# Performance work log

Measured on AMD Instinct MI355X. Metric: run time of the kernel, lower is better.

The kernel has to match this reference:

```python
import jax, jax.numpy as jnp
import numpy as np

INPUT_DIM, LATENT_DIM, HIDDEN_DIM, BATCH = 1024, 128, 1024, 32768


def setup_inputs() -> dict:
    key = jax.random.key(0)
    ks = jax.random.split(key, 12)
    s = 0.02
    x = (jax.random.uniform(ks[0], (BATCH, INPUT_DIM)) < 0.5).astype(jnp.float32)  # binary data
    eps = jax.random.normal(ks[1], (BATCH, LATENT_DIM), dtype=jnp.float32)
    return {
        "x": x,
        "eps": eps,
        "We1": jax.random.normal(ks[2], (INPUT_DIM, HIDDEN_DIM)) * s,
        "be1": jnp.zeros((HIDDEN_DIM,), jnp.float32),
        "Wmu": jax.random.normal(ks[3], (HIDDEN_DIM, LATENT_DIM)) * s,
        "bmu": jnp.zeros((LATENT_DIM,), jnp.float32),
        "Wls": jax.random.normal(ks[4], (HIDDEN_DIM, LATENT_DIM)) * s,
        "bls": jnp.zeros((LATENT_DIM,), jnp.float32),
        "Wd1": jax.random.normal(ks[5], (LATENT_DIM, HIDDEN_DIM)) * s,
        "bd1": jnp.zeros((HIDDEN_DIM,), jnp.float32),
        "Wd2": jax.random.normal(ks[6], (HIDDEN_DIM, INPUT_DIM)) * s,
        "bd2": jnp.zeros((INPUT_DIM,), jnp.float32),
    }


def reference(x, eps, We1, be1, Wmu, bmu, Wls, bls, Wd1, bd1, Wd2, bd2):
    # Encoder: one hidden ReLU layer, mu / logsigma heads
    h = jax.nn.relu(x @ We1 + be1)                      # [B, H]
    mu = h @ Wmu + bmu                                  # [B, L]
    logsigma = h @ Wls + bls                            # [B, L]
    # Reparameterization: z = sigma * eps + mu (vectorized diag(exp(logsigma)) @ eps)
    z = mu + jnp.exp(logsigma) * eps                    # [B, L]
    # Decoder: one hidden ReLU layer, sigmoid Bernoulli params
    hd = jax.nn.relu(z @ Wd1 + bd1)                     # [B, H]
    theta = jax.nn.sigmoid(hd @ Wd2 + bd2)              # [B, D]
    # Bernoulli log-likelihood: sum_j log(theta^x * (1-theta)^(1-x))
    log_px = jnp.sum(x * jnp.log(theta) + (1.0 - x) * jnp.log1p(-theta), axis=-1)  # [B]
    # KL(q||N(0,I)) = 0.5 * sum(sigma^2 + mu^2 - log(sigma^2) - 1)
    kl = 0.5 * jnp.sum(jnp.exp(2.0 * logsigma) + mu * mu - 2.0 * logsigma - 1.0, axis=-1)  # [B]
    return log_px - kl                                  # elbo_mc [B]
```

## Files before the change

### kernel.cpp

```cpp
#include <hip/hip_runtime.h>
#include <cstdint>
#include <cstddef>


typedef __bf16 bf16x8 __attribute__((ext_vector_type(8)));
typedef float f32x4 __attribute__((ext_vector_type(4)));

__device__ __forceinline__ unsigned short f32_to_bf16(float f) {
  unsigned int u = __float_as_uint(f);
  u += 0x7fffu + ((u >> 16) & 1u);
  return (unsigned short)(u >> 16);
}

struct TransJob { const float* in; unsigned short* out; int K, N, blkEnd; };

__global__ void prep_k(TransJob j0, TransJob j1, TransJob j2,
                       TransJob j3, TransJob j4,
                       const float* __restrict__ x,
                       unsigned short* __restrict__ xbf,
                       unsigned short* __restrict__ xbit,
                       int n4, int castBlocks) {
  __shared__ float tile[32][33];
  int bid = blockIdx.x;
  int tx = threadIdx.x, ty = threadIdx.y;
  if (bid >= j4.blkEnd) {
    int tid = ty * 32 + tx;
    int stride = castBlocks * 256;
    for (int i = (bid - j4.blkEnd) * 256 + tid; i < n4; i += stride) {
      float4 v = reinterpret_cast<const float4*>(x)[i];
      ushort4 o = make_ushort4(f32_to_bf16(v.x), f32_to_bf16(v.y),
                               f32_to_bf16(v.z), f32_to_bf16(v.w));
      reinterpret_cast<ushort4*>(xbf)[i] = o;
      unsigned int nib = (v.x != 0.f ? 1u : 0u) | (v.y != 0.f ? 2u : 0u) |
                         (v.z != 0.f ? 4u : 0u) | (v.w != 0.f ? 8u : 0u);
      unsigned int n1 = __shfl_down(nib, 1, 64);
      unsigned int n2 = __shfl_down(nib, 2, 64);
      unsigned int n3 = __shfl_down(nib, 3, 64);
      if ((tid & 3) == 0)
        xbit[i >> 2] = (unsigned short)(nib | (n1 << 4) | (n2 << 8) | (n3 << 12));
    }
    return;
  }
  TransJob j; int base;
  if (bid < j0.blkEnd)      { j = j0; base = 0; }
  else if (bid < j1.blkEnd) { j = j1; base = j0.blkEnd; }
  else if (bid < j2.blkEnd) { j = j2; base = j1.blkEnd; }
  else if (bid < j3.blkEnd) { j = j3; base = j2.blkEnd; }
  else                      { j = j4; base = j3.blkEnd; }
  int local = bid - base;
  int gxN = j.N >> 5;
  int n0 = (local % gxN) * 32, k0 = (local / gxN) * 32;
#pragma unroll
  for (int r = 0; r < 32; r += 8)
    tile[ty + r][tx] = j.in[(size_t)(k0 + ty + r) * j.N + n0 + tx];
  __syncthreads();
#pragma unroll
  for (int r = 0; r < 32; r += 8)
    j.out[(size_t)(n0 + ty + r) * j.K + k0 + tx] = f32_to_bf16(tile[tx][ty + r]);
}

__device__ __forceinline__ void gl_lds16(const unsigned short* g, unsigned short* l) {
  __builtin_amdgcn_global_load_lds(
      (__attribute__((address_space(1))) void*)g,
      (__attribute__((address_space(3))) void*)l, 16, 0, 0);
}

template <int EPI, int TAG>
__global__ __launch_bounds__(512, 2) void gemm256(
    const unsigned short* __restrict__ A, const unsigned short* __restrict__ BT,
    int gx, int N, int K,
    const float* __restrict__ bias0,
    unsigned short* __restrict__ outb, float* __restrict__ outf,
    const unsigned short* __restrict__ xbit) {
  __shared__ __align__(16) unsigned short lds[2][2][256 * 64];

  const int tid = threadIdx.x;
  const int lane = tid & 63;
  const int wave = tid >> 6;
  const int wr = wave >> 2;
  const int wc = wave & 3;
  const int lm = lane & 15, lq = lane >> 4;
  const int sw = lm & 7;

  const int bid = blockIdx.x;
  const int xcd = bid & 7;
  const int t8 = bid >> 3;
  const int m0 = (xcd + 8 * (t8 / gx)) * 256;
  const int n0 = (t8 % gx) * 256;
  const int NT = K >> 6;

  const unsigned short* gpA[2];
  const unsigned short* gpB[2];
  int loA[2], loB[2];
#pragma unroll
  for (int r = 0; r < 2; ++r) {
    int c = tid + 512 * r, rl = c >> 3, q8 = c & 7;
    int rowA = (rl & 63) + ((rl >> 6) << 7);
    int rowB = (rl & 31) + ((rl >> 5) << 6);
    gpA[r] = A + (size_t)(m0 + rowA) * K + (q8 ^ (rowA & 7)) * 8;
    gpB[r] = BT + (size_t)(n0 + rowB) * K + (q8 ^ (rowB & 7)) * 8;
    loA[r] = rowA * 64 + q8 * 8;
    loB[r] = rowB * 64 + q8 * 8;
  }

  auto stage = [&](int kind, int buf, int kt) {
#pragma unroll
    for (int r = 0; r < 2; ++r) {
      if (kind == 0)      gl_lds16(gpA[r] + kt * 64,          &lds[buf][0][loA[r]]);
      else if (kind == 3) gl_lds16(gpA[r] + 64 * K + kt * 64, &lds[buf][0][loA[r] + 64 * 64]);
      else if (kind == 1) gl_lds16(gpB[r] + kt * 64,          &lds[buf][1][loB[r]]);
      else                gl_lds16(gpB[r] + 32 * K + kt * 64, &lds[buf][1][loB[r] + 32 * 64]);
    }
  };

  stage(0, 0, 0); stage(1, 0, 0); stage(2, 0, 0); stage(3, 0, 0);
  stage(0, 1, 1); stage(1, 1, 1); stage(2, 1, 1);
  asm volatile("s_waitcnt vmcnt(6)" ::: "memory");
  __builtin_amdgcn_s_barrier();

  f32x4 acc[8][4] = {};

  const int aRow = (wr * 128 + lm) * 64;
  const int bRow = (wc * 64 + lm) * 64;
  const int c0 = ((0 | lq) ^ sw) * 8;
  const int c1 = ((4 | lq) ^ sw) * 8;

  for (int t = 0; t < NT; ++t) {
    const int b = t & 1;
    const unsigned short* Ab = &lds[b][0][0];
    const unsigned short* Bb = &lds[b][1][0];
    bf16x8 af[4][2], bf1[2][2], bf2[2][2];

#pragma unroll
    for (int i = 0; i < 4; ++i) {
      af[i][0] = *reinterpret_cast<const bf16x8*>(Ab + aRow + i * 1024 + c0);
      af[i][1] = *reinterpret_cast<const bf16x8*>(Ab + aRow + i * 1024 + c1);
    }
#pragma unroll
    for (int j = 0; j < 2; ++j) {
      bf1[j][0] = *reinterpret_cast<const bf16x8*>(Bb + bRow + j * 1024 + c0);
      bf1[j][1] = *reinterpret_cast<const bf16x8*>(Bb + bRow + j * 1024 + c1);
    }
    if (t + 1 < NT) stage(3, (t + 1) & 1, t + 1);
    __builtin_amdgcn_s_barrier();
    asm volatile("s_waitcnt lgkmcnt(0)" ::: "memory");
    __builtin_amdgcn_sched_barrier(0);
    __builtin_amdgcn_s_setprio(1);
#pragma unroll
    for (int s = 0; s < 2; ++s)
#pragma unroll
      for (int i = 0; i < 4; ++i)
#pragma unroll
        for (int j = 0; j < 2; ++j)
          acc[i][j] = __builtin_amdgcn_mfma_f32_16x16x32_bf16(af[i][s], bf1[j][s], acc[i][j], 0, 0, 0);
    __builtin_amdgcn_s_setprio(0);
    __builtin_amdgcn_s_barrier();

#pragma unroll
    for (int j = 0; j < 2; ++j) {
      bf2[j][0] = *reinterpret_cast<const bf16x8*>(Bb + bRow + (j + 2) * 1024 + c0);
      bf2[j][1] = *reinterpret_cast<const bf16x8*>(Bb + bRow + (j + 2) * 1024 + c1);
    }
    if (t + 2 < NT) stage(0, b, t + 2);
    __builtin_amdgcn_s_barrier();
    asm volatile("s_waitcnt lgkmcnt(0)" ::: "memory");
    __builtin_amdgcn_sched_barrier(0);
    __builtin_amdgcn_s_setprio(1);
#pragma unroll
    for (int s = 0; s < 2; ++s)
#pragma unroll
      for (int i = 0; i < 4; ++i)
#pragma unroll
        for (int j = 0; j < 2; ++j)
          acc[i][j + 2] = __builtin_amdgcn_mfma_f32_16x16x32_bf16(af[i][s], bf2[j][s], acc[i][j + 2], 0, 0, 0);
    __builtin_amdgcn_s_setprio(0);
    __builtin_amdgcn_s_barrier();

#pragma unroll
    for (int i = 0; i < 4; ++i) {
      af[i][0] = *reinterpret_cast<const bf16x8*>(Ab + aRow + (64 + i * 16) * 64 + c0);
      af[i][1] = *reinterpret_cast<const bf16x8*>(Ab + aRow + (64 + i * 16) * 64 + c1);
    }
    if (t + 2 < NT) stage(1, b, t + 2);
    __builtin_amdgcn_s_barrier();
    asm volatile("s_waitcnt lgkmcnt(0)" ::: "memory");
    __builtin_amdgcn_sched_barrier(0);
    __builtin_amdgcn_s_setprio(1);
#pragma unroll
    for (int s = 0; s < 2; ++s)
#pragma unroll
      for (int i = 0; i < 4; ++i)
#pragma unroll
        for (int j = 0; j < 2; ++j)
          acc[i + 4][j] = __builtin_amdgcn_mfma_f32_16x16x32_bf16(af[i][s], bf1[j][s], acc[i + 4][j], 0, 0, 0);
    __builtin_amdgcn_s_setprio(0);
    __builtin_amdgcn_s_barrier();

    if (t + 2 < NT) stage(2, b, t + 2);
    __builtin_amdgcn_s_barrier();
    __builtin_amdgcn_s_setprio(1);
#pragma unroll
    for (int s = 0; s < 2; ++s)
#pragma unroll
      for (int i = 0; i < 4; ++i)
#pragma unroll
        for (int j = 0; j < 2; ++j)
          acc[i + 4][j + 2] = __builtin_amdgcn_mfma_f32_16x16x32_bf16(af[i][s], bf2[j][s], acc[i + 4][j + 2], 0, 0, 0);
    __builtin_amdgcn_s_setprio(0);
    if (t + 2 < NT)      { asm volatile("s_waitcnt vmcnt(6)" ::: "memory"); }
    else if (t + 1 < NT) { asm volatile("s_waitcnt vmcnt(0)" ::: "memory"); }
    __builtin_amdgcn_s_barrier();
  }

  if (EPI == 0) {
#pragma unroll
    for (int i = 0; i < 8; ++i)
#pragma unroll
      for (int j = 0; j < 4; ++j) {
        int col = n0 + wc * 64 + j * 16 + lm;
        float bias = bias0[col];
#pragma unroll
        for (int r = 0; r < 4; ++r) {
          int row = m0 + wr * 128 + i * 16 + lq * 4 + r;
          float v = acc[i][j][r] + bias;
          outb[(size_t)row * N + col] = f32_to_bf16(fmaxf(v, 0.f));
        }
      }
  } else {
    const int wpr = N >> 4;
#pragma unroll
    for (int i = 0; i < 8; ++i) {
      float rs[4] = {0.f, 0.f, 0.f, 0.f};
#pragma unroll
      for (int j = 0; j < 4; ++j) {
        int col = n0 + wc * 64 + j * 16 + lm;
        float bias = bias0[col];
        int w16 = (col >> 4);
#pragma unroll
        for (int r = 0; r < 4; ++r) {
          int row = m0 + wr * 128 + i * 16 + lq * 4 + r;
          float l = acc[i][j][r] + bias;
          unsigned short mask = xbit[(size_t)row * wpr + w16];
          float tt = ((mask >> lm) & 1) ? -l : l;
          float sp = fmaxf(tt, 0.f) + __logf(1.f + __expf(-fabsf(tt)));
          rs[r] -= sp;
        }
      }
#pragma unroll
      for (int off = 1; off < 16; off <<= 1)
#pragma unroll
        for (int r = 0; r < 4; ++r) rs[r] += __shfl_xor(rs[r], off, 64);
      if (lm == 0) {
#pragma unroll
        for (int r = 0; r < 4; ++r)
          atomicAdd(&outf[m0 + wr * 128 + i * 16 + lq * 4 + r], rs[r]);
      }
    }
  }
}

__global__ __launch_bounds__(256, 1) void latent_fused(
    const unsigned short* A,
    const unsigned short* __restrict__ BT,
    const unsigned short* __restrict__ WD1,
    const float* __restrict__ bmu, const float* __restrict__ bls,
    const float* __restrict__ bd1,
    const float* __restrict__ eps,
    unsigned short* hd,
    float* __restrict__ out) {
  __shared__ __align__(16) unsigned short smem[65536];
  unsigned short* As0 = smem;
  unsigned short* As1 = smem + 8192;
  unsigned short* Bs0 = smem + 16384;
  unsigned short* Bs1 = smem + 32768;
  unsigned short* zs  = smem + 49152;
  unsigned short* Bs2 = smem;

  const int K = 1024;
  const int tid = threadIdx.x;
  const int lane = tid & 63;
  const int wave = tid >> 6;
  const int m0 = blockIdx.x * 128;
  const int lm = lane & 15, lq = lane >> 4;
  const int sw = lm & 7;

  const unsigned short* agp[4];
  const unsigned short* bgp[8];
#pragma unroll
  for (int r = 0; r < 4; ++r) {
    int c = tid + 256 * r;
    int row = c >> 3, q = (c & 7) ^ (row & 7);
    agp[r] = A + (size_t)(m0 + row) * K + q * 8;
  }
#pragma unroll
  for (int r = 0; r < 8; ++r) {
    int c = tid + 256 * r;
    int row = c >> 3, q = (c & 7) ^ (row & 7);
    bgp[r] = BT + (size_t)row * K + q * 8;
  }

  auto stage1 = [&](int buf, int kt) {
    unsigned short* Ad = buf ? As1 : As0;
    unsigned short* Bd = buf ? Bs1 : Bs0;
#pragma unroll
    for (int r = 0; r < 4; ++r) gl_lds16(agp[r] + kt, Ad + (tid + 256 * r) * 8);
#pragma unroll
    for (int r = 0; r < 8; ++r) gl_lds16(bgp[r] + kt, Bd + (tid + 256 * r) * 8);
  };

  f32x4 acc[2][16] = {};

  stage1(0, 0);
  __syncthreads();

  for (int t = 0; t < 16; ++t) {
    const int cur = t & 1;
    if (t + 1 < 16) stage1(cur ^ 1, (t + 1) * 64);
    const unsigned short* Ab = cur ? As1 : As0;
    const unsigned short* Bb = cur ? Bs1 : Bs0;
#pragma unroll
    for (int s = 0; s < 2; ++s) {
      const int so = ((s << 2) | lq) ^ sw;
      bf16x8 af[2];
#pragma unroll
      for (int i = 0; i < 2; ++i)
        af[i] = *reinterpret_cast<const bf16x8*>(Ab + (wave * 32 + i * 16 + lm) * 64 + so * 8);
#pragma unroll
      for (int j = 0; j < 16; ++j) {
        bf16x8 b = *reinterpret_cast<const bf16x8*>(Bb + (j * 16 + lm) * 64 + so * 8);
        acc[0][j] = __builtin_amdgcn_mfma_f32_16x16x32_bf16(af[0], b, acc[0][j], 0, 0, 0);
        acc[1][j] = __builtin_amdgcn_mfma_f32_16x16x32_bf16(af[1], b, acc[1][j], 0, 0, 0);
      }
    }
    __syncthreads();
  }

  auto stage2 = [&](int nt) {
#pragma unroll
    for (int ri = 0; ri < 16; ++ri) {
      int c = tid + 256 * ri;
      int row = c >> 4, slot = c & 15;
      int gc = slot ^ (row & 7);
      gl_lds16(WD1 + (size_t)(nt * 256 + row) * 128 + gc * 8, Bs2 + c * 8);
    }
  };
  stage2(0);

#pragma unroll
  for (int i = 0; i < 2; ++i) {
    float kl[4] = {0.f, 0.f, 0.f, 0.f};
#pragma unroll
    for (int j = 0; j < 8; ++j) {
      int dim = j * 16 + lm;
      float bm = bmu[dim], bl = bls[dim];
#pragma unroll
      for (int r = 0; r < 4; ++r) {
        int rowl = wave * 32 + i * 16 + lq * 4 + r;
        float mu = acc[i][j][r] + bm;
        float ls = acc[i][j + 8][r] + bl;
        float e = eps[(size_t)(m0 + rowl) * 128 + dim];
        float zv = fmaf(__expf(ls), e, mu);
        int chunk = (dim >> 3);
        int slot = chunk ^ (rowl & 7);
        zs[rowl * 128 + slot * 8 + (lm & 7)] = f32_to_bf16(zv);
        kl[r] += 0.5f * (__expf(2.f * ls) + mu * mu - 2.f * ls - 1.f);
      }
    }
#pragma unroll
    for (int off = 1; off < 16; off <<= 1)
#pragma unroll
      for (int r = 0; r < 4; ++r) kl[r] += __shfl_xor(kl[r], off, 64);
    if (lm == 0) {
#pragma unroll
      for (int r = 0; r < 4; ++r)
        out[m0 + wave * 32 + i * 16 + lq * 4 + r] = -kl[r];
    }
  }

  for (int nt = 0; nt < 4; ++nt) {
    asm volatile("s_waitcnt vmcnt(0)" ::: "memory");
    __syncthreads();
    f32x4 acc2[2][16] = {};
#pragma unroll
    for (int ks = 0; ks < 4; ++ks) {
      const int cks = (ks * 4 + lq) ^ (lm & 7);
      bf16x8 a0 = *reinterpret_cast<const bf16x8*>(zs + (wave * 32 + lm) * 128 + cks * 8);
      bf16x8 a1 = *reinterpret_cast<const bf16x8*>(zs + (wave * 32 + 16 + lm) * 128 + cks * 8);
#pragma unroll
      for (int j = 0; j < 16; ++j) {
        bf16x8 b = *reinterpret_cast<const bf16x8*>(Bs2 + (j * 16 + lm) * 128 + cks * 8);
        acc2[0][j] = __builtin_amdgcn_mfma_f32_16x16x32_bf16(a0, b, acc2[0][j], 0, 0, 0);
        acc2[1][j] = __builtin_amdgcn_mfma_f32_16x16x32_bf16(a1, b, acc2[1][j], 0, 0, 0);
      }
    }
    __syncthreads();
    if (nt + 1 < 4) stage2(nt + 1);
#pragma unroll
    for (int i = 0; i < 2; ++i)
#pragma unroll
      for (int j = 0; j < 16; ++j) {
        int col = nt * 256 + j * 16 + lm;
        float bias = bd1[col];
#pragma unroll
        for (int r = 0; r < 4; ++r) {
          int row = m0 + wave * 32 + i * 16 + lq * 4 + r;
          float v = acc2[i][j][r] + bias;
          hd[(size_t)row * 1024 + col] = f32_to_bf16(fmaxf(v, 0.f));
        }
      }
  }
}

extern "C" void kernel_launch(void* const* d_in, const int* in_sizes, int n_in,
                              void* d_out, int out_size, void* d_ws, size_t ws_size,
                              hipStream_t stream) {
  const float* x   = (const float*)d_in[0];
  const float* eps = (const float*)d_in[1];
  const float* We1 = (const float*)d_in[2];
  const float* be1 = (const float*)d_in[3];
  const float* Wmu = (const float*)d_in[4];
  const float* bmu = (const float*)d_in[5];
  const float* Wls = (const float*)d_in[6];
  const float* bls = (const float*)d_in[7];
  const float* Wd1 = (const float*)d_in[8];
  const float* bd1 = (const float*)d_in[9];
  const float* Wd2 = (const float*)d_in[10];
  const float* bd2 = (const float*)d_in[11];
  float* out = (float*)d_out;

  const int B = 32768, D = 1024, H = 1024, L = 128;

  char* ws = (char*)d_ws;
  size_t off = 0;
  auto alloc = [&](size_t bytes) {
    void* p = ws + off;
    off += (bytes + 255) & ~(size_t)255;
    return p;
  };
  unsigned short* xbf  = (unsigned short*)alloc((size_t)B * D * 2);
  unsigned short* xbit = (unsigned short*)alloc((size_t)B * D / 8);
  unsigned short* w1t  = (unsigned short*)alloc((size_t)H * D * 2);
  unsigned short* w2t  = (unsigned short*)alloc((size_t)256 * H * 2);
  unsigned short* wd1t = (unsigned short*)alloc((size_t)H * L * 2);
  unsigned short* wd2t = (unsigned short*)alloc((size_t)D * H * 2);
  unsigned short* h    = (unsigned short*)alloc((size_t)B * H * 2);
  unsigned short* hd   = h;

  TransJob j0{We1, w1t, D, H, 1024};
  TransJob j1{Wmu, w2t, H, L, 1152};
  TransJob j2{Wls, w2t + 128 * H, H, L, 1280};
  TransJob j3{Wd1, wd1t, L, H, 1408};
  TransJob j4{Wd2, wd2t, H, D, 2432};
  prep_k<<<2432 + 2048, dim3(32, 8), 0, stream>>>(
      j0, j1, j2, j3, j4, x, xbf, xbit, B * D / 4, 2048);

  gemm256<0, 1><<<512, 512, 0, stream>>>(
      xbf, w1t, 4, H, D, be1, h, nullptr, nullptr);
  latent_fused<<<B / 128, 256, 0, stream>>>(
      h, w2t, wd1t, bmu, bls, bd1, eps, hd, out);
  gemm256<2, 4><<<512, 512, 0, stream>>>(
      hd, wd2t, 4, D, H, bd2, nullptr, out, xbit);

  (void)in_sizes; (void)n_in; (void)out_size; (void)ws_size;
}
```

Before: 440.8 us.

## Expand bit-packed input in LDS for first GEMM instead of bf16 copy

The prep kernel no longer writes a bf16 copy of x. The first encoder GEMM instead loads the bit-packed x tile (one bit per element) into LDS once per block and expands it to bf16 0/1 values in shared memory each k-step. This removes a 64MB bf16 write plus its re-read, leaving only the compact bitmask traffic. The cost is ALU and LDS-store work for expansion inside the main loop, a single A buffer with changed wait counts, and an encoding that is only exact because x is binary.

```diff
diff --git a/kernel.cpp b/kernel.cpp
--- a/kernel.cpp
+++ b/kernel.cpp
@@ -17,7 +17,6 @@
 __global__ void prep_k(TransJob j0, TransJob j1, TransJob j2,
                        TransJob j3, TransJob j4,
                        const float* __restrict__ x,
-                       unsigned short* __restrict__ xbf,
                        unsigned short* __restrict__ xbit,
                        int n4, int castBlocks) {
   __shared__ float tile[32][33];
@@ -28,9 +27,6 @@
     int stride = castBlocks * 256;
     for (int i = (bid - j4.blkEnd) * 256 + tid; i < n4; i += stride) {
       float4 v = reinterpret_cast<const float4*>(x)[i];
-      ushort4 o = make_ushort4(f32_to_bf16(v.x), f32_to_bf16(v.y),
-                               f32_to_bf16(v.z), f32_to_bf16(v.w));
-      reinterpret_cast<ushort4*>(xbf)[i] = o;
       unsigned int nib = (v.x != 0.f ? 1u : 0u) | (v.y != 0.f ? 2u : 0u) |
                          (v.z != 0.f ? 4u : 0u) | (v.w != 0.f ? 8u : 0u);
       unsigned int n1 = __shfl_down(nib, 1, 64);
@@ -65,14 +61,14 @@
       (__attribute__((address_space(3))) void*)l, 16, 0, 0);
 }
 
-template <int EPI, int TAG>
+template <int EPI, int TAG, int ABIT>
 __global__ __launch_bounds__(512, 2) void gemm256(
     const unsigned short* __restrict__ A, const unsigned short* __restrict__ BT,
     int gx, int N, int K,
     const float* __restrict__ bias0,
     unsigned short* __restrict__ outb, float* __restrict__ outf,
     const unsigned short* __restrict__ xbit) {
-  __shared__ __align__(16) unsigned short lds[2][2][256 * 64];
+  __shared__ __align__(16) unsigned short smem[65536];
 
   const int tid = threadIdx.x;
   const int lane = tid & 63;
@@ -89,34 +85,75 @@
   const int n0 = (t8 % gx) * 256;
   const int NT = K >> 6;
 
+  unsigned short* const smemp = smem;
+  auto Abuf = [&](int b) -> unsigned short* {
+    return ABIT ? smemp : smemp + b * 32768;
+  };
+  auto Bbuf = [&](int b) -> unsigned short* {
+    return ABIT ? smemp + 16384 + b * 16384 : smemp + b * 32768 + 16384;
+  };
+
   const unsigned short* gpA[2];
   const unsigned short* gpB[2];
-  int loA[2], loB[2];
+  int loA[2], loB[2], xaddr[2];
 #pragma unroll
   for (int r = 0; r < 2; ++r) {
     int c = tid + 512 * r, rl = c >> 3, q8 = c & 7;
     int rowA = (rl & 63) + ((rl >> 6) << 7);
     int rowB = (rl & 31) + ((rl >> 5) << 6);
-    gpA[r] = A + (size_t)(m0 + rowA) * K + (q8 ^ (rowA & 7)) * 8;
+    int qgA = q8 ^ (rowA & 7);
+    gpA[r] = A + (size_t)(m0 + rowA) * K + qgA * 8;
     gpB[r] = BT + (size_t)(n0 + rowB) * K + (q8 ^ (rowB & 7)) * 8;
     loA[r] = rowA * 64 + q8 * 8;
     loB[r] = rowB * 64 + q8 * 8;
+    xaddr[r] = rowA * 128 + qgA;
   }
 
   auto stage = [&](int kind, int buf, int kt) {
 #pragma unroll
     for (int r = 0; r < 2; ++r) {
-      if (kind == 0)      gl_lds16(gpA[r] + kt * 64,          &lds[buf][0][loA[r]]);
-      else if (kind == 3) gl_lds16(gpA[r] + 64 * K + kt * 64, &lds[buf][0][loA[r] + 64 * 64]);
-      else if (kind == 1) gl_lds16(gpB[r] + kt * 64,          &lds[buf][1][loB[r]]);
-      else                gl_lds16(gpB[r] + 32 * K + kt * 64, &lds[buf][1][loB[r] + 32 * 64]);
-    }
-  };
-
-  stage(0, 0, 0); stage(1, 0, 0); stage(2, 0, 0); stage(3, 0, 0);
-  stage(0, 1, 1); stage(1, 1, 1); stage(2, 1, 1);
-  asm volatile("s_waitcnt vmcnt(6)" ::: "memory");
-  __builtin_amdgcn_s_barrier();
+      if (kind == 0)      { if (!ABIT) gl_lds16(gpA[r] + kt * 64,          Abuf(buf) + loA[r]); }
+      else if (kind == 3) { if (!ABIT) gl_lds16(gpA[r] + 64 * K + kt * 64, Abuf(buf) + loA[r] + 4096); }
+      else if (kind == 1) gl_lds16(gpB[r] + kt * 64,          Bbuf(buf) + loB[r]);
+      else                gl_lds16(gpB[r] + 32 * K + kt * 64, Bbuf(buf) + loB[r] + 2048);
+    }
+  };
+
+  auto expandA = [&](int t) {
+    const unsigned char* xsb = reinterpret_cast<const unsigned char*>(smemp + 49152);
+    unsigned short* As = smemp;
+#pragma unroll
+    for (int r = 0; r < 2; ++r) {
+#pragma unroll
+      for (int h = 0; h < 2; ++h) {
+        unsigned int b = xsb[xaddr[r] + h * 8192 + 8 * t];
+        unsigned int o0 = ((b & 1u)        ? 0x3F80u : 0u) | ((b & 2u)   ? 0x3F800000u : 0u);
+        unsigned int o1 = (((b >> 2) & 1u) ? 0x3F80u : 0u) | ((b & 8u)   ? 0x3F800000u : 0u);
+        unsigned int o2 = (((b >> 4) & 1u) ? 0x3F80u : 0u) | ((b & 32u)  ? 0x3F800000u : 0u);
+        unsigned int o3 = (((b >> 6) & 1u) ? 0x3F80u : 0u) | ((b & 128u) ? 0x3F800000u : 0u);
+        *reinterpret_cast<uint4*>(As + loA[r] + h * 4096) = make_uint4(o0, o1, o2, o3);
+      }
+    }
+  };
+
+  if (ABIT) {
+    const unsigned short* xp = xbit + (size_t)m0 * 64;
+    unsigned short* xs = smemp + 49152;
+#pragma unroll
+    for (int i = 0; i < 4; ++i)
+      gl_lds16(xp + (tid + 512 * i) * 8, xs + (tid + 512 * i) * 8);
+    stage(1, 0, 0); stage(2, 0, 0);
+    stage(1, 1, 1); stage(2, 1, 1);
+    asm volatile("s_waitcnt vmcnt(8)" ::: "memory");
+    expandA(0);
+    asm volatile("s_waitcnt vmcnt(4) lgkmcnt(0)" ::: "memory");
+    __builtin_amdgcn_s_barrier();
+  } else {
+    stage(0, 0, 0); stage(1, 0, 0); stage(2, 0, 0); stage(3, 0, 0);
+    stage(0, 1, 1); stage(1, 1, 1); stage(2, 1, 1);
+    asm volatile("s_waitcnt vmcnt(6)" ::: "memory");
+    __builtin_amdgcn_s_barrier();
+  }
 
   f32x4 acc[8][4] = {};
 
@@ -127,8 +164,8 @@
 
   for (int t = 0; t < NT; ++t) {
     const int b = t & 1;
-    const unsigned short* Ab = &lds[b][0][0];
-    const unsigned short* Bb = &lds[b][1][0];
+    const unsigned short* Ab = Abuf(b);
+    const unsigned short* Bb = Bbuf(b);
     bf16x8 af[4][2], bf1[2][2], bf2[2][2];
 
 #pragma unroll
@@ -141,7 +178,7 @@
       bf1[j][0] = *reinterpret_cast<const bf16x8*>(Bb + bRow + j * 1024 + c0);
       bf1[j][1] = *reinterpret_cast<const bf16x8*>(Bb + bRow + j * 1024 + c1);
     }
-    if (t + 1 < NT) stage(3, (t + 1) & 1, t + 1);
+    if (!ABIT && t + 1 < NT) stage(3, (t + 1) & 1, t + 1);
     __builtin_amdgcn_s_barrier();
     asm volatile("s_waitcnt lgkmcnt(0)" ::: "memory");
     __builtin_amdgcn_sched_barrier(0);
@@ -161,7 +198,7 @@
       bf2[j][0] = *reinterpret_cast<const bf16x8*>(Bb + bRow + (j + 2) * 1024 + c0);
       bf2[j][1] = *reinterpret_cast<const bf16x8*>(Bb + bRow + (j + 2) * 1024 + c1);
     }
-    if (t + 2 < NT) stage(0, b, t + 2);
+    if (t + 2 < NT) stage(ABIT ? 1 : 0, b, t + 2);
     __builtin_amdgcn_s_barrier();
     asm volatile("s_waitcnt lgkmcnt(0)" ::: "memory");
     __builtin_amdgcn_sched_barrier(0);
@@ -181,7 +218,7 @@
       af[i][0] = *reinterpret_cast<const bf16x8*>(Ab + aRow + (64 + i * 16) * 64 + c0);
       af[i][1] = *reinterpret_cast<const bf16x8*>(Ab + aRow + (64 + i * 16) * 64 + c1);
     }
-    if (t + 2 < NT) stage(1, b, t + 2);
+    if (t + 2 < NT) stage(ABIT ? 2 : 1, b, t + 2);
     __builtin_amdgcn_s_barrier();
     asm volatile("s_waitcnt lgkmcnt(0)" ::: "memory");
     __builtin_amdgcn_sched_barrier(0);
@@ -196,7 +233,8 @@
     __builtin_amdgcn_s_setprio(0);
     __builtin_amdgcn_s_barrier();
 
-    if (t + 2 < NT) stage(2, b, t + 2);
+    if (ABIT) { if (t + 1 < NT) expandA(t + 1); }
+    else      { if (t + 2 < NT) stage(2, b, t + 2); }
     __builtin_amdgcn_s_barrier();
     __builtin_amdgcn_s_setprio(1);
 #pragma unroll
@@ -207,8 +245,13 @@
         for (int j = 0; j < 2; ++j)
           acc[i + 4][j + 2] = __builtin_amdgcn_mfma_f32_16x16x32_bf16(af[i][s], bf2[j][s], acc[i + 4][j + 2], 0, 0, 0);
     __builtin_amdgcn_s_setprio(0);
-    if (t + 2 < NT)      { asm volatile("s_waitcnt vmcnt(6)" ::: "memory"); }
-    else if (t + 1 < NT) { asm volatile("s_waitcnt vmcnt(0)" ::: "memory"); }
+    if (ABIT) {
+      if (t + 2 < NT) { asm volatile("s_waitcnt vmcnt(4) lgkmcnt(0)" ::: "memory"); }
+      else            { asm volatile("s_waitcnt vmcnt(0) lgkmcnt(0)" ::: "memory"); }
+    } else {
+      if (t + 2 < NT)      { asm volatile("s_waitcnt vmcnt(6)" ::: "memory"); }
+      else if (t + 1 < NT) { asm volatile("s_waitcnt vmcnt(0)" ::: "memory"); }
+    }
     __builtin_amdgcn_s_barrier();
   }
 
@@ -437,7 +480,6 @@
     off += (bytes + 255) & ~(size_t)255;
     return p;
   };
-  unsigned short* xbf  = (unsigned short*)alloc((size_t)B * D * 2);
   unsigned short* xbit = (unsigned short*)alloc((size_t)B * D / 8);
   unsigned short* w1t  = (unsigned short*)alloc((size_t)H * D * 2);
   unsigned short* w2t  = (unsigned short*)alloc((size_t)256 * H * 2);
@@ -452,13 +494,13 @@
   TransJob j3{Wd1, wd1t, L, H, 1408};
   TransJob j4{Wd2, wd2t, H, D, 2432};
   prep_k<<<2432 + 2048, dim3(32, 8), 0, stream>>>(
-      j0, j1, j2, j3, j4, x, xbf, xbit, B * D / 4, 2048);
-
-  gemm256<0, 1><<<512, 512, 0, stream>>>(
-      xbf, w1t, 4, H, D, be1, h, nullptr, nullptr);
+      j0, j1, j2, j3, j4, x, xbit, B * D / 4, 2048);
+
+  gemm256<0, 1, 1><<<512, 512, 0, stream>>>(
+      nullptr, w1t, 4, H, D, be1, h, nullptr, xbit);
   latent_fused<<<B / 128, 256, 0, stream>>>(
       h, w2t, wd1t, bmu, bls, bd1, eps, hd, out);
-  gemm256<2, 4><<<512, 512, 0, stream>>>(
+  gemm256<2, 4, 0><<<512, 512, 0, stream>>>(
       hd, wd2t, 4, D, H, bd2, nullptr, out, xbit);
 
   (void)in_sizes; (void)n_in; (void)out_size; (void)ws_size;
```

New measurement: 438.5 us. No clear change (-0.5%).
